# Optimization experiments

Measured on AMD Instinct MI355X. Metric: run time of the kernel, lower is better.

The kernel has to match this reference:

```python
import jax, jax.numpy as jnp
import numpy as np

N_NODES = 100000
N_EDGES = 1600000
F_IN = 256
F_OUT = 128


def setup_inputs() -> dict:
    key = jax.random.key(0)
    k1, k2, k3, k4, k5 = jax.random.split(key, 5)
    x = jax.random.normal(k1, (N_NODES, F_IN), dtype=jnp.float32)
    edge_src = jax.random.randint(k2, (N_EDGES,), 0, N_NODES, dtype=jnp.int64)
    edge_dst = jax.random.randint(k3, (N_EDGES,), 0, N_NODES, dtype=jnp.int64)
    edge_vals = jax.random.uniform(k4, (N_EDGES,), dtype=jnp.float32)
    kernel = jax.random.normal(k5, (F_IN, F_OUT), dtype=jnp.float32) * (1.0 / np.sqrt(F_IN))
    bias = jnp.zeros((F_OUT,), dtype=jnp.float32)
    return {"x": x, "edge_src": edge_src, "edge_dst": edge_dst,
            "edge_vals": edge_vals, "kernel": kernel, "bias": bias}


def reference(x, edge_src, edge_dst, edge_vals, kernel, bias):
    # h = x @ kernel  (dense feature transform), [N, F_OUT]
    h = x @ kernel
    # output = adj @ h  (sparse aggregation over COO edges)
    # message for edge e: adj[dst, src] * h[src]
    msg = h[edge_src] * edge_vals[:, None]          # [E, F_OUT]
    out = jax.ops.segment_sum(msg, edge_dst, num_segments=N_NODES)
    return out + bias
```

## Files before the change

### kernel.cpp

```cpp
#include <hip/hip_runtime.h>

constexpr int F_IN  = 256;
constexpr int F_OUT = 128;

constexpr int BSHIFT = 6;
constexpr int BUCKET = 1 << BSHIFT;
constexpr int SUPSH  = 5;
constexpr int MAXNB  = 2048;
constexpr int EPT    = 16;
constexpr int BATCH  = 256 * EPT;
constexpr int BPS    = 8;

typedef __attribute__((ext_vector_type(8))) short short8;
typedef __attribute__((ext_vector_type(4))) float f32x4;

__device__ __forceinline__ unsigned short f2bf(float f) {
    unsigned u = __float_as_uint(f);
    u += 0x7fffu + ((u >> 16) & 1u);
    return (unsigned short)(u >> 16);
}

__global__ void prep_wt_kernel(const float* __restrict__ W,
                               unsigned short* __restrict__ Wt)
{
    int n = blockIdx.x;
    int k = threadIdx.x;
    int ks = k >> 5, kk = k & 31;
    Wt[((ks * F_OUT) + n) * 32 + kk] = f2bf(W[k * F_OUT + n]);
}

#define BS_LD 40

__global__ __launch_bounds__(256) void gemm_mfma_kernel(
    const float* __restrict__ x, const unsigned short* __restrict__ Wt,
    unsigned short* __restrict__ h, int n_nodes)
{
    __shared__ unsigned short Bs[F_OUT * BS_LD];

    const int tid  = threadIdx.x;
    const int wave = tid >> 6;
    const int lane = tid & 63;
    const int m16  = lane & 15;
    const int quad = lane >> 4;
    const int k0q  = quad * 8;
    const int arow = blockIdx.x * 64 + wave * 16 + m16;
    const bool inb = arow < n_nodes;

    f32x4 acc[8];
    #pragma unroll
    for (int t = 0; t < 8; ++t) acc[t] = (f32x4)(0.f);

    float4 a0 = make_float4(0.f,0.f,0.f,0.f), a1 = a0;
    if (inb) {
        a0 = *(const float4*)&x[(long long)arow * F_IN + k0q];
        a1 = *(const float4*)&x[(long long)arow * F_IN + k0q + 4];
    }

    for (int ks = 0; ks < 8; ++ks) {
        const uint4* wsrc = (const uint4*)(Wt + (size_t)ks * F_OUT * 32);
        #pragma unroll
        for (int p = 0; p < 2; ++p) {
            int c   = p * 256 + tid;
            int row = c >> 2;
            int o16 = c & 3;
            *(uint4*)&Bs[row * BS_LD + o16 * 8] = wsrc[c];
        }
        __syncthreads();

        short8 af;
        af[0] = (short)f2bf(a0.x); af[1] = (short)f2bf(a0.y);
        af[2] = (short)f2bf(a0.z); af[3] = (short)f2bf(a0.w);
        af[4] = (short)f2bf(a1.x); af[5] = (short)f2bf(a1.y);
        af[6] = (short)f2bf(a1.z); af[7] = (short)f2bf(a1.w);
        if (!inb) af = (short8)0;

        if (ks < 7 && inb) {
            int kn = (ks + 1) * 32 + k0q;
            a0 = *(const float4*)&x[(long long)arow * F_IN + kn];
            a1 = *(const float4*)&x[(long long)arow * F_IN + kn + 4];
        }

        #pragma unroll
        for (int t = 0; t < 8; ++t) {
            int n = t * 16 + m16;
            short8 bf = *(const short8*)&Bs[n * BS_LD + k0q];
            acc[t] = __builtin_amdgcn_mfma_f32_16x16x32_bf16(af, bf, acc[t], 0, 0, 0);
        }
        __syncthreads();
    }

    const int rbase = blockIdx.x * 64 + wave * 16 + quad * 4;
    #pragma unroll
    for (int r = 0; r < 4; ++r) {
        int grow = rbase + r;
        if (grow < n_nodes) {
            #pragma unroll
            for (int t = 0; t < 8; ++t)
                h[(long long)grow * F_OUT + t * 16 + m16] = f2bf(acc[t][r]);
        }
    }
}

__global__ __launch_bounds__(256) void hist_kernel(
    const int* __restrict__ dst, int* __restrict__ cnt, int n_edges, int nb)
{
    __shared__ int hs[MAXNB];
    const int tid = threadIdx.x;
    for (int i = tid; i < nb; i += 256) hs[i] = 0;
    __syncthreads();
    for (int i = blockIdx.x * 256 + tid; i < n_edges; i += gridDim.x * 256)
        atomicAdd(&hs[dst[i] >> BSHIFT], 1);
    __syncthreads();
    for (int i = tid; i < nb; i += 256) {
        int v = hs[i];
        if (v) atomicAdd(&cnt[i], v);
    }
}

__global__ __launch_bounds__(1024) void scan_kernel(
    const int* __restrict__ cnt, int* __restrict__ bucket_start,
    int* __restrict__ super_start, int* __restrict__ cursorA,
    int* __restrict__ cursorB, int nb, int nsup)
{
    __shared__ int s[1024];
    int t = threadIdx.x;
    int b0 = 2 * t, b1 = 2 * t + 1;
    int c0 = (b0 < nb) ? cnt[b0] : 0;
    int c1 = (b1 < nb) ? cnt[b1] : 0;
    s[t] = c0 + c1;
    __syncthreads();
    for (int off = 1; off < 1024; off <<= 1) {
        int tmp = (t >= off) ? s[t - off] : 0;
        __syncthreads();
        s[t] += tmp;
        __syncthreads();
    }
    int run = s[t] - (c0 + c1);
    if (b0 < nb) { bucket_start[b0] = run; cursorB[b0] = run; }
    run += c0;
    if (b1 < nb) { bucket_start[b1] = run; cursorB[b1] = run; }
    if (t == 1023) bucket_start[nb] = s[1023];
    __syncthreads();
    for (int i = t; i <= nsup; i += 1024) {
        int k = i << SUPSH;
        int v = (k < nb) ? bucket_start[k] : bucket_start[nb];
        super_start[i] = v;
        if (i < nsup) cursorA[i] = v;
    }
}

__global__ __launch_bounds__(256) void partition_a_kernel(
    const int* __restrict__ src, const int* __restrict__ dst,
    const float* __restrict__ vals, int* __restrict__ cursorA,
    uint2* __restrict__ payA, int n_edges)
{
    __shared__ int hist[64];
    __shared__ int base[64];
    const int tid = threadIdx.x;
    const int i0  = blockIdx.x * BATCH;

    if (tid < 64) hist[tid] = 0;
    __syncthreads();

    uint2 p[EPT];
    int   sb[EPT];
    int   rk[EPT];
    #pragma unroll
    for (int j = 0; j < EPT; ++j) {
        int i = i0 + j * 256 + tid;
        sb[j] = -1;
        if (i < n_edges) {
            int d = dst[i];
            p[j] = make_uint2((unsigned)src[i] | ((unsigned)(d & 2047) << 17),
                              __float_as_uint(vals[i]));
            sb[j] = d >> (BSHIFT + SUPSH);
            rk[j] = atomicAdd(&hist[sb[j]], 1);
        }
    }
    __syncthreads();
    if (tid < 64) { int v = hist[tid]; if (v) base[tid] = atomicAdd(&cursorA[tid], v); }
    __syncthreads();
    #pragma unroll
    for (int j = 0; j < EPT; ++j)
        if (sb[j] >= 0) payA[base[sb[j]] + rk[j]] = p[j];
}

__global__ __launch_bounds__(256) void partition_b_kernel(
    const uint2* __restrict__ payA, const int* __restrict__ super_start,
    int* __restrict__ cursorB, uint2* __restrict__ payload)
{
    __shared__ int hist[32];
    __shared__ int base[32];
    const int sp  = blockIdx.x / BPS;
    const int sub = blockIdx.x % BPS;
    const int lo  = super_start[sp];
    const int hi  = super_start[sp + 1];
    const int slice = (hi - lo + BPS - 1) / BPS;
    const int start = lo + sub * slice;
    const int end   = min(start + slice, hi);
    const int tid = threadIdx.x;

    for (int b = start; b < end; b += BATCH) {
        if (tid < 32) hist[tid] = 0;
        __syncthreads();
        uint2 p[EPT];
        int   fb[EPT];
        int   rk[EPT];
        #pragma unroll
        for (int j = 0; j < EPT; ++j) {
            int i = b + j * 256 + tid;
            fb[j] = -1;
            if (i < end) {
                p[j] = payA[i];
                fb[j] = (p[j].x >> 23) & 31;
                rk[j] = atomicAdd(&hist[fb[j]], 1);
            }
        }
        __syncthreads();
        if (tid < 32) {
            int v = hist[tid];
            if (v) base[tid] = atomicAdd(&cursorB[(sp << SUPSH) + tid], v);
        }
        __syncthreads();
        #pragma unroll
        for (int j = 0; j < EPT; ++j)
            if (fb[j] >= 0) {
                unsigned xf = (p[j].x & 0x1FFFFu) | (((p[j].x >> 17) & 63u) << 24);
                payload[base[fb[j]] + rk[j]] = make_uint2(xf, p[j].y);
            }
        __syncthreads();
    }
}

__global__ __launch_bounds__(256) void local_sort_kernel(
    const uint2* __restrict__ payload, const int* __restrict__ bucket_start,
    uint2* __restrict__ sorted, int* __restrict__ offsets, int n_nodes)
{
    __shared__ int bins[BUCKET];
    __shared__ int bcur[BUCKET];

    const int b   = blockIdx.x;
    const int tid = threadIdx.x;
    const int start = bucket_start[b];
    const int end   = bucket_start[b + 1];

    if (tid < BUCKET) bins[tid] = 0;
    __syncthreads();

    for (int e = start + tid; e < end; e += 256)
        atomicAdd(&bins[payload[e].x >> 24], 1);
    __syncthreads();

    if (tid == 0) {
        int run = start;
        for (int i = 0; i < BUCKET; ++i) { bcur[i] = run; run += bins[i]; }
    }
    __syncthreads();

    if (tid < BUCKET) {
        int node = (b << BSHIFT) + tid;
        if (node < n_nodes) offsets[node] = bcur[tid];
    }
    __syncthreads();

    for (int e = start + tid; e < end; e += 256) {
        uint2 p = payload[e];
        int pos = atomicAdd(&bcur[p.x >> 24], 1);
        sorted[pos] = p;
    }
}

__global__ __launch_bounds__(256) void gather_kernel(
    const unsigned short* __restrict__ h, const int* __restrict__ offsets,
    const uint2* __restrict__ sv, const float* __restrict__ bias,
    float* __restrict__ out, int n_nodes, int n_edges)
{
    int node = blockIdx.x * 4 + (threadIdx.x >> 6);
    if (node >= n_nodes) return;
    int lane = threadIdx.x & 63;
    int f = lane * 2;

    int start = offsets[node];
    int end   = (node + 1 < n_nodes) ? offsets[node + 1] : n_edges;

    float ax = 0.f, ay = 0.f;

    for (int e = start; e < end; e += 16) {
        uint2 p[16];
        #pragma unroll
        for (int j = 0; j < 16; ++j) {
            int ei = (e + j < end) ? e + j : end - 1;
            p[j] = sv[ei];
        }
        unsigned u[16];
        #pragma unroll
        for (int j = 0; j < 16; ++j)
            u[j] = *(const unsigned*)&h[(size_t)(p[j].x & 0x00FFFFFFu) * F_OUT + f];
        #pragma unroll
        for (int j = 0; j < 16; ++j) {
            float v = (e + j < end) ? __uint_as_float(p[j].y) : 0.f;
            ax += v * __uint_as_float(u[j] << 16);
            ay += v * __uint_as_float(u[j] & 0xffff0000u);
        }
    }

    float2 b = *(const float2*)&bias[f];
    *(float2*)&out[(size_t)node * F_OUT + f] = make_float2(ax + b.x, ay + b.y);
}

extern "C" void kernel_launch(void* const* d_in, const int* in_sizes, int n_in,
                              void* d_out, int out_size, void* d_ws, size_t ws_size,
                              hipStream_t stream)
{
    const float* x     = (const float*)d_in[0];
    const int*   esrc  = (const int*)d_in[1];
    const int*   edst  = (const int*)d_in[2];
    const float* evals = (const float*)d_in[3];
    const float* W     = (const float*)d_in[4];
    const float* bias  = (const float*)d_in[5];
    float*       out   = (float*)d_out;

    const int n_nodes = in_sizes[0] / F_IN;
    const int n_edges = in_sizes[1];
    const int nb      = (n_nodes + BUCKET - 1) >> BSHIFT;
    const int nsup    = (nb + (1 << SUPSH) - 1) >> SUPSH;

    auto align16 = [](size_t v) { return (v + 15) & ~(size_t)15; };
    char*  base = (char*)d_ws;
    size_t off  = 0;
    unsigned short* h  = (unsigned short*)(base + off); off = align16(off + (size_t)n_nodes * F_OUT * 2);
    unsigned short* Wt = (unsigned short*)(base + off); off = align16(off + (size_t)F_IN * F_OUT * 2);
    int*   cnt          = (int*)(base + off);   off = align16(off + (size_t)nb * 4);
    int*   bucket_start = (int*)(base + off);   off = align16(off + (size_t)(nb + 1) * 4);
    int*   super_start  = (int*)(base + off);   off = align16(off + (size_t)(nsup + 1) * 4);
    int*   cursorA      = (int*)(base + off);   off = align16(off + (size_t)nsup * 4);
    int*   cursorB      = (int*)(base + off);   off = align16(off + (size_t)nb * 4);
    int*   offsets      = (int*)(base + off);   off = align16(off + (size_t)n_nodes * 4);
    uint2* payA         = (uint2*)(base + off); off = align16(off + (size_t)n_edges * 8);
    uint2* payload      = (uint2*)(base + off); off = align16(off + (size_t)n_edges * 8);
    uint2* sorted       = payA;
    (void)ws_size;

    prep_wt_kernel<<<F_OUT, F_IN, 0, stream>>>(W, Wt);
    gemm_mfma_kernel<<<(n_nodes + 63) / 64, 256, 0, stream>>>(x, Wt, h, n_nodes);

    hipMemsetAsync(cnt, 0, (size_t)nb * 4, stream);
    hist_kernel<<<256, 256, 0, stream>>>(edst, cnt, n_edges, nb);
    scan_kernel<<<1, 1024, 0, stream>>>(cnt, bucket_start, super_start,
                                        cursorA, cursorB, nb, nsup);
    partition_a_kernel<<<(n_edges + BATCH - 1) / BATCH, 256, 0, stream>>>(
        esrc, edst, evals, cursorA, payA, n_edges);
    partition_b_kernel<<<nsup * BPS, 256, 0, stream>>>(
        payA, super_start, cursorB, payload);

    local_sort_kernel<<<nb, 256, 0, stream>>>(
        payload, bucket_start, sorted, offsets, n_nodes);
    gather_kernel<<<(n_nodes + 3) / 4, 256, 0, stream>>>(
        h, offsets, sorted, bias, out, n_nodes, n_edges);
}
```

Before: 358.2 us.

## Collapse two-level edge partition into one super-bucket counting sort per block

```diff
diff --git a/kernel.cpp b/kernel.cpp
--- a/kernel.cpp
+++ b/kernel.cpp
@@ -4,12 +4,11 @@
 constexpr int F_OUT = 128;
 
 constexpr int BSHIFT = 6;
-constexpr int BUCKET = 1 << BSHIFT;
 constexpr int SUPSH  = 5;
-constexpr int MAXNB  = 2048;
+constexpr int NPSH   = BSHIFT + SUPSH;
+constexpr int NPS    = 1 << NPSH;
 constexpr int EPT    = 16;
 constexpr int BATCH  = 256 * EPT;
-constexpr int BPS    = 8;
 
 typedef __attribute__((ext_vector_type(8))) short short8;
 typedef __attribute__((ext_vector_type(4))) float f32x4;
@@ -21,12 +20,14 @@
 }
 
 __global__ void prep_wt_kernel(const float* __restrict__ W,
-                               unsigned short* __restrict__ Wt)
+                               unsigned short* __restrict__ Wt,
+                               int* __restrict__ cnt)
 {
     int n = blockIdx.x;
     int k = threadIdx.x;
     int ks = k >> 5, kk = k & 31;
     Wt[((ks * F_OUT) + n) * 32 + kk] = f2bf(W[k * F_OUT + n]);
+    if (blockIdx.x == 0 && threadIdx.x < 64) cnt[threadIdx.x] = 0;
 }
 
 #define BS_LD 40
@@ -35,7 +36,7 @@
     const float* __restrict__ x, const unsigned short* __restrict__ Wt,
     unsigned short* __restrict__ h, int n_nodes)
 {
-    __shared__ unsigned short Bs[F_OUT * BS_LD];
+    __shared__ unsigned short Bs[2][F_OUT * BS_LD];
 
     const int tid  = threadIdx.x;
     const int wave = tid >> 6;
@@ -50,22 +51,30 @@
     #pragma unroll
     for (int t = 0; t < 8; ++t) acc[t] = (f32x4)(0.f);
 
+    {
+        const uint4* wsrc = (const uint4*)Wt;
+        #pragma unroll
+        for (int p = 0; p < 2; ++p) {
+            int c = p * 256 + tid;
+            *(uint4*)&Bs[0][(c >> 2) * BS_LD + (c & 3) * 8] = wsrc[c];
+        }
+    }
+
     float4 a0 = make_float4(0.f,0.f,0.f,0.f), a1 = a0;
     if (inb) {
         a0 = *(const float4*)&x[(long long)arow * F_IN + k0q];
         a1 = *(const float4*)&x[(long long)arow * F_IN + k0q + 4];
     }
-
+    __syncthreads();
+
+    #pragma unroll
     for (int ks = 0; ks < 8; ++ks) {
-        const uint4* wsrc = (const uint4*)(Wt + (size_t)ks * F_OUT * 32);
-        #pragma unroll
-        for (int p = 0; p < 2; ++p) {
-            int c   = p * 256 + tid;
-            int row = c >> 2;
-            int o16 = c & 3;
-            *(uint4*)&Bs[row * BS_LD + o16 * 8] = wsrc[c];
-        }
-        __syncthreads();
+        uint4 s0, s1;
+        if (ks < 7) {
+            const uint4* wsrc = (const uint4*)(Wt + (size_t)(ks + 1) * F_OUT * 32);
+            s0 = wsrc[tid];
+            s1 = wsrc[256 + tid];
+        }
 
         short8 af;
         af[0] = (short)f2bf(a0.x); af[1] = (short)f2bf(a0.y);
@@ -83,10 +92,16 @@
         #pragma unroll
         for (int t = 0; t < 8; ++t) {
             int n = t * 16 + m16;
-            short8 bf = *(const short8*)&Bs[n * BS_LD + k0q];
+            short8 bf = *(const short8*)&Bs[ks & 1][n * BS_LD + k0q];
             acc[t] = __builtin_amdgcn_mfma_f32_16x16x32_bf16(af, bf, acc[t], 0, 0, 0);
         }
-        __syncthreads();
+
+        if (ks < 7) {
+            *(uint4*)&Bs[(ks + 1) & 1][(tid >> 2) * BS_LD + (tid & 3) * 8] = s0;
+            int c1 = 256 + tid;
+            *(uint4*)&Bs[(ks + 1) & 1][(c1 >> 2) * BS_LD + (c1 & 3) * 8] = s1;
+            __syncthreads();
+        }
     }
 
     const int rbase = blockIdx.x * 64 + wave * 16 + quad * 4;
@@ -102,50 +117,35 @@
 }
 
 __global__ __launch_bounds__(256) void hist_kernel(
-    const int* __restrict__ dst, int* __restrict__ cnt, int n_edges, int nb)
-{
-    __shared__ int hs[MAXNB];
+    const int* __restrict__ dst, int* __restrict__ cnt, int n_edges)
+{
+    __shared__ int hs[64];
     const int tid = threadIdx.x;
-    for (int i = tid; i < nb; i += 256) hs[i] = 0;
+    if (tid < 64) hs[tid] = 0;
     __syncthreads();
     for (int i = blockIdx.x * 256 + tid; i < n_edges; i += gridDim.x * 256)
-        atomicAdd(&hs[dst[i] >> BSHIFT], 1);
-    __syncthreads();
-    for (int i = tid; i < nb; i += 256) {
-        int v = hs[i];
-        if (v) atomicAdd(&cnt[i], v);
-    }
-}
-
-__global__ __launch_bounds__(1024) void scan_kernel(
-    const int* __restrict__ cnt, int* __restrict__ bucket_start,
-    int* __restrict__ super_start, int* __restrict__ cursorA,
-    int* __restrict__ cursorB, int nb, int nsup)
-{
-    __shared__ int s[1024];
+        atomicAdd(&hs[dst[i] >> NPSH], 1);
+    __syncthreads();
+    if (tid < 64) {
+        int v = hs[tid];
+        if (v) atomicAdd(&cnt[tid], v);
+    }
+}
+
+__global__ void scan_sup_kernel(const int* __restrict__ cnt,
+                                int* __restrict__ super_start,
+                                int* __restrict__ cursorA, int nsup)
+{
+    __shared__ int s[64];
     int t = threadIdx.x;
-    int b0 = 2 * t, b1 = 2 * t + 1;
-    int c0 = (b0 < nb) ? cnt[b0] : 0;
-    int c1 = (b1 < nb) ? cnt[b1] : 0;
-    s[t] = c0 + c1;
-    __syncthreads();
-    for (int off = 1; off < 1024; off <<= 1) {
-        int tmp = (t >= off) ? s[t - off] : 0;
-        __syncthreads();
-        s[t] += tmp;
-        __syncthreads();
-    }
-    int run = s[t] - (c0 + c1);
-    if (b0 < nb) { bucket_start[b0] = run; cursorB[b0] = run; }
-    run += c0;
-    if (b1 < nb) { bucket_start[b1] = run; cursorB[b1] = run; }
-    if (t == 1023) bucket_start[nb] = s[1023];
-    __syncthreads();
-    for (int i = t; i <= nsup; i += 1024) {
-        int k = i << SUPSH;
-        int v = (k < nb) ? bucket_start[k] : bucket_start[nb];
-        super_start[i] = v;
-        if (i < nsup) cursorA[i] = v;
+    s[t] = (t < nsup) ? cnt[t] : 0;
+    __syncthreads();
+    if (t == 0) {
+        int run = 0;
+        for (int i = 0; i < nsup; ++i) {
+            super_start[i] = run; cursorA[i] = run; run += s[i];
+        }
+        super_start[nsup] = run;
     }
 }
 
@@ -171,9 +171,9 @@
         sb[j] = -1;
         if (i < n_edges) {
             int d = dst[i];
-            p[j] = make_uint2((unsigned)src[i] | ((unsigned)(d & 2047) << 17),
+            p[j] = make_uint2((unsigned)src[i] | ((unsigned)(d & (NPS - 1)) << 17),
                               __float_as_uint(vals[i]));
-            sb[j] = d >> (BSHIFT + SUPSH);
+            sb[j] = d >> NPSH;
             rk[j] = atomicAdd(&hist[sb[j]], 1);
         }
     }
@@ -185,88 +185,80 @@
         if (sb[j] >= 0) payA[base[sb[j]] + rk[j]] = p[j];
 }
 
-__global__ __launch_bounds__(256) void partition_b_kernel(
+__global__ __launch_bounds__(512) void sort_super_kernel(
     const uint2* __restrict__ payA, const int* __restrict__ super_start,
-    int* __restrict__ cursorB, uint2* __restrict__ payload)
-{
-    __shared__ int hist[32];
-    __shared__ int base[32];
-    const int sp  = blockIdx.x / BPS;
-    const int sub = blockIdx.x % BPS;
+    uint2* __restrict__ sorted, int* __restrict__ offsets, int n_nodes)
+{
+    __shared__ int bins[NPS];
+    __shared__ int bcur[NPS];
+    __shared__ int ss[512];
+
+    const int sp  = blockIdx.x;
+    const int tid = threadIdx.x;
     const int lo  = super_start[sp];
     const int hi  = super_start[sp + 1];
-    const int slice = (hi - lo + BPS - 1) / BPS;
-    const int start = lo + sub * slice;
-    const int end   = min(start + slice, hi);
-    const int tid = threadIdx.x;
-
-    for (int b = start; b < end; b += BATCH) {
-        if (tid < 32) hist[tid] = 0;
+
+    for (int i = tid; i < NPS; i += 512) bins[i] = 0;
+    __syncthreads();
+
+    {
+        int e = lo + tid;
+        for (; e + 3 * 512 < hi; e += 4 * 512) {
+            unsigned x0 = payA[e].x, x1 = payA[e + 512].x,
+                     x2 = payA[e + 1024].x, x3 = payA[e + 1536].x;
+            atomicAdd(&bins[(x0 >> 17) & (NPS - 1)], 1);
+            atomicAdd(&bins[(x1 >> 17) & (NPS - 1)], 1);
+            atomicAdd(&bins[(x2 >> 17) & (NPS - 1)], 1);
+            atomicAdd(&bins[(x3 >> 17) & (NPS - 1)], 1);
+        }
+        for (; e < hi; e += 512)
+            atomicAdd(&bins[(payA[e].x >> 17) & (NPS - 1)], 1);
+    }
+    __syncthreads();
+
+    const int b4 = tid * 4;
+    int c0 = bins[b4], c1 = bins[b4 + 1], c2 = bins[b4 + 2], c3 = bins[b4 + 3];
+    int tot = c0 + c1 + c2 + c3;
+    ss[tid] = tot;
+    __syncthreads();
+    for (int off = 1; off < 512; off <<= 1) {
+        int v = (tid >= off) ? ss[tid - off] : 0;
         __syncthreads();
-        uint2 p[EPT];
-        int   fb[EPT];
-        int   rk[EPT];
-        #pragma unroll
-        for (int j = 0; j < EPT; ++j) {
-            int i = b + j * 256 + tid;
-            fb[j] = -1;
-            if (i < end) {
-                p[j] = payA[i];
-                fb[j] = (p[j].x >> 23) & 31;
-                rk[j] = atomicAdd(&hist[fb[j]], 1);
-            }
-        }
+        ss[tid] += v;
         __syncthreads();
-        if (tid < 32) {
-            int v = hist[tid];
-            if (v) base[tid] = atomicAdd(&cursorB[(sp << SUPSH) + tid], v);
-        }
-        __syncthreads();
-        #pragma unroll
-        for (int j = 0; j < EPT; ++j)
-            if (fb[j] >= 0) {
-                unsigned xf = (p[j].x & 0x1FFFFu) | (((p[j].x >> 17) & 63u) << 24);
-                payload[base[fb[j]] + rk[j]] = make_uint2(xf, p[j].y);
-            }
-        __syncthreads();
-    }
-}
-
-__global__ __launch_bounds__(256) void local_sort_kernel(
-    const uint2* __restrict__ payload, const int* __restrict__ bucket_start,
-    uint2* __restrict__ sorted, int* __restrict__ offsets, int n_nodes)
-{
-    __shared__ int bins[BUCKET];
-    __shared__ int bcur[BUCKET];
-
-    const int b   = blockIdx.x;
-    const int tid = threadIdx.x;
-    const int start = bucket_start[b];
-    const int end   = bucket_start[b + 1];
-
-    if (tid < BUCKET) bins[tid] = 0;
-    __syncthreads();
-
-    for (int e = start + tid; e < end; e += 256)
-        atomicAdd(&bins[payload[e].x >> 24], 1);
-    __syncthreads();
-
-    if (tid == 0) {
-        int run = start;
-        for (int i = 0; i < BUCKET; ++i) { bcur[i] = run; run += bins[i]; }
-    }
-    __syncthreads();
-
-    if (tid < BUCKET) {
-        int node = (b << BSHIFT) + tid;
-        if (node < n_nodes) offsets[node] = bcur[tid];
-    }
-    __syncthreads();
-
-    for (int e = start + tid; e < end; e += 256) {
-        uint2 p = payload[e];
-        int pos = atomicAdd(&bcur[p.x >> 24], 1);
-        sorted[pos] = p;
+    }
+    int run = lo + ss[tid] - tot;
+    bcur[b4]     = run;
+    bcur[b4 + 1] = run + c0;
+    bcur[b4 + 2] = run + c0 + c1;
+    bcur[b4 + 3] = run + c0 + c1 + c2;
+    __syncthreads();
+
+    const int node0 = sp << NPSH;
+    for (int i = tid; i < NPS; i += 512) {
+        int nd = node0 + i;
+        if (nd < n_nodes) offsets[nd] = bcur[i];
+    }
+    __syncthreads();
+
+    {
+        int e = lo + tid;
+        for (; e + 3 * 512 < hi; e += 4 * 512) {
+            uint2 p0 = payA[e], p1 = payA[e + 512], p2 = payA[e + 1024], p3 = payA[e + 1536];
+            int q0 = atomicAdd(&bcur[(p0.x >> 17) & (NPS - 1)], 1);
+            int q1 = atomicAdd(&bcur[(p1.x >> 17) & (NPS - 1)], 1);
+            int q2 = atomicAdd(&bcur[(p2.x >> 17) & (NPS - 1)], 1);
+            int q3 = atomicAdd(&bcur[(p3.x >> 17) & (NPS - 1)], 1);
+            sorted[q0] = make_uint2(p0.x & 0x1FFFFu, p0.y);
+            sorted[q1] = make_uint2(p1.x & 0x1FFFFu, p1.y);
+            sorted[q2] = make_uint2(p2.x & 0x1FFFFu, p2.y);
+            sorted[q3] = make_uint2(p3.x & 0x1FFFFu, p3.y);
+        }
+        for (; e < hi; e += 512) {
+            uint2 p = payA[e];
+            int q = atomicAdd(&bcur[(p.x >> 17) & (NPS - 1)], 1);
+            sorted[q] = make_uint2(p.x & 0x1FFFFu, p.y);
+        }
     }
 }
 
@@ -322,39 +314,31 @@
 
     const int n_nodes = in_sizes[0] / F_IN;
     const int n_edges = in_sizes[1];
-    const int nb      = (n_nodes + BUCKET - 1) >> BSHIFT;
-    const int nsup    = (nb + (1 << SUPSH) - 1) >> SUPSH;
+    const int nsup    = (n_nodes + NPS - 1) >> NPSH;
 
     auto align16 = [](size_t v) { return (v + 15) & ~(size_t)15; };
     char*  base = (char*)d_ws;
     size_t off  = 0;
     unsigned short* h  = (unsigned short*)(base + off); off = align16(off + (size_t)n_nodes * F_OUT * 2);
     unsigned short* Wt = (unsigned short*)(base + off); off = align16(off + (size_t)F_IN * F_OUT * 2);
-    int*   cnt          = (int*)(base + off);   off = align16(off + (size_t)nb * 4);
-    int*   bucket_start = (int*)(base + off);   off = align16(off + (size_t)(nb + 1) * 4);
-    int*   super_start  = (int*)(base + off);   off = align16(off + (size_t)(nsup + 1) * 4);
-    int*   cursorA      = (int*)(base + off);   off = align16(off + (size_t)nsup * 4);
-    int*   cursorB      = (int*)(base + off);   off = align16(off + (size_t)nb * 4);
-    int*   offsets      = (int*)(base + off);   off = align16(off + (size_t)n_nodes * 4);
-    uint2* payA         = (uint2*)(base + off); off = align16(off + (size_t)n_edges * 8);
-    uint2* payload      = (uint2*)(base + off); off = align16(off + (size_t)n_edges * 8);
-    uint2* sorted       = payA;
+    int*   cnt         = (int*)(base + off);   off = align16(off + (size_t)64 * 4);
+    int*   super_start = (int*)(base + off);   off = align16(off + (size_t)(nsup + 1) * 4);
+    int*   cursorA     = (int*)(base + off);   off = align16(off + (size_t)64 * 4);
+    int*   offsets     = (int*)(base + off);   off = align16(off + (size_t)n_nodes * 4);
+    uint2* payA        = (uint2*)(base + off); off = align16(off + (size_t)n_edges * 8);
+    uint2* sorted      = (uint2*)(base + off); off = align16(off + (size_t)n_edges * 8);
     (void)ws_size;
 
-    prep_wt_kernel<<<F_OUT, F_IN, 0, stream>>>(W, Wt);
+    prep_wt_kernel<<<F_OUT, F_IN, 0, stream>>>(W, Wt, cnt);
     gemm_mfma_kernel<<<(n_nodes + 63) / 64, 256, 0, stream>>>(x, Wt, h, n_nodes);
 
-    hipMemsetAsync(cnt, 0, (size_t)nb * 4, stream);
-    hist_kernel<<<256, 256, 0, stream>>>(edst, cnt, n_edges, nb);
-    scan_kernel<<<1, 1024, 0, stream>>>(cnt, bucket_start, super_start,
-                                        cursorA, cursorB, nb, nsup);
+    hist_kernel<<<256, 256, 0, stream>>>(edst, cnt, n_edges);
+    scan_sup_kernel<<<1, 64, 0, stream>>>(cnt, super_start, cursorA, nsup);
     partition_a_kernel<<<(n_edges + BATCH - 1) / BATCH, 256, 0, stream>>>(
         esrc, edst, evals, cursorA, payA, n_edges);
-    partition_b_kernel<<<nsup * BPS, 256, 0, stream>>>(
-        payA, super_start, cursorB, payload);
-
-    local_sort_kernel<<<nb, 256, 0, stream>>>(
-        payload, bucket_start, sorted, offsets, n_nodes);
+    sort_super_kernel<<<nsup, 512, 0, stream>>>(
+        payA, super_start, sorted, offsets, n_nodes);
+
     gather_kernel<<<(n_nodes + 3) / 4, 256, 0, stream>>>(
         h, offsets, sorted, bias, out, n_nodes, n_edges);
 }
```

Result: no change. 359.7 us (+0.4%).
